# Optimization experiments

Hardware: AMD Instinct MI355X
Metric: run time of the kernel (lower is better)

The kernel has to match this reference:

```python
import jax, jax.numpy as jnp
import numpy as np

PI = np.float32(np.pi)


def _normal(v):
    return v / jnp.linalg.norm(v, axis=-1, keepdims=True)


def camera_mats(cameras):
    # cameras: [V,5] -> rotation matrices c: [V,3,3], camera origins o: [V,3]
    theta = cameras[:, 0] * (PI / 180.0)
    phi = cameras[:, 1] * (PI / 180.0)
    camy = cameras[:, 3] * jnp.sin(phi)
    lens = cameras[:, 3] * jnp.cos(phi)
    camx = lens * jnp.cos(theta)
    camz = lens * jnp.sin(theta)
    Zax = jnp.stack([camx, camy, camz], -1)                                   # [V,3]
    Yax = jnp.stack([camy * jnp.cos(theta + PI), lens, camy * jnp.sin(theta + PI)], -1)
    Xax = jnp.cross(Yax, Zax)
    c = jnp.stack([_normal(Xax), _normal(Yax), _normal(Zax)], axis=1)         # [V,3,3]
    return c, Zax


def setup_inputs() -> dict:
    key = jax.random.key(0)
    k0, k1, k2, k3, k4, k5 = jax.random.split(key, 6)
    N = 65536
    return {
        "inputs": jax.random.normal(k0, (N, 3), jnp.float32),
        "cameras": jax.random.uniform(k1, (3, 5), jnp.float32),
        "feat0": jax.random.normal(k2, (3, 64, 56, 56), jnp.float32),
        "feat1": jax.random.normal(k3, (3, 128, 28, 28), jnp.float32),
        "feat2": jax.random.normal(k4, (3, 256, 14, 14), jnp.float32),
        "feat3": jax.random.normal(k5, (3, 512, 7, 7), jnp.float32),
    }


def reference(inputs, cameras, feat0, feat1, feat2, feat3):
    V = 3
    N = inputs.shape[0]
    c, o = camera_mats(cameras)                      # [V,3,3], [V,3]
    # camera_trans_inv with view 0: xyz @ inv(c0.T) + o0
    point_origin = inputs @ jnp.linalg.inv(c[0].T) + o[0]          # [N,3]
    # camera_trans per view: (p - o_v) @ c_v.T
    pts = jnp.einsum('vnd,vkd->vnk', point_origin[None, :, :] - o[:, None, :], c)  # [V,N,3]
    X, Y, Z = pts[..., 0], pts[..., 1], pts[..., 2]
    h = jnp.clip(jnp.nan_to_num(248.0 * (-Y) / (-Z) + 112.0), 0.0, 223.0)
    w = jnp.clip(jnp.nan_to_num(248.0 * X / (-Z) + 112.0), 0.0, 223.0)
    n = jnp.broadcast_to(jnp.arange(V, dtype=jnp.float32)[:, None], (V, N))
    indices = jnp.stack([n, h, w], axis=-1)                        # [V,N,3] float

    def gather(feat, size):
        # faithful: n is also divided and truncated -> batch index always 0
        idx = (indices / (224.0 / size)).astype(jnp.int32)         # [V,N,3]
        f = jnp.transpose(feat, (0, 2, 3, 1))                      # [B,H,W,C]
        return f[idx[..., 0], idx[..., 1], idx[..., 2]]            # [V,N,C]

    image_feature = jnp.concatenate(
        [gather(feat0, 56.0), gather(feat1, 28.0), gather(feat2, 14.0), gather(feat3, 7.0)],
        axis=2)                                                    # [V,N,960]
    fmax = jnp.max(image_feature, axis=0)
    fmean = jnp.mean(image_feature, axis=0)
    fstd = jnp.sqrt(jnp.mean((image_feature - fmean) ** 2, axis=0))  # biased std
    return jnp.concatenate([inputs, fmax, fmean, fstd], axis=1)    # [N, 3+3*960]
```

## Files before the change

kernel.cpp:

```cpp
#include <hip/hip_runtime.h>
#include <math.h>


#define TBL_TOTAL 376320
#define TBL_OFF0  0
#define TBL_OFF1  200704
#define TBL_OFF2  301056
#define TBL_OFF3  351232

__device__ __forceinline__ void compute_cams(const float* __restrict__ cams,
                                             double M[3][3], double o0[3],
                                             double cm[3][3][3], double om[3][3]) {
  const double DEG  = (double)(3.14159274101257324f / 180.0f);
  const double PI_D = (double)3.14159274101257324f;
  for (int v = 0; v < 3; ++v) {
    double th = (double)cams[v * 5 + 0] * DEG;
    double ph = (double)cams[v * 5 + 1] * DEG;
    double dd = (double)cams[v * 5 + 3];
    double camy = dd * sin(ph);
    double lens = dd * cos(ph);
    double camx = lens * cos(th);
    double camz = lens * sin(th);
    double Zx = camx, Zy = camy, Zz = camz;
    double Yx = camy * cos(th + PI_D), Yy = lens, Yz = camy * sin(th + PI_D);
    double Xx = Yy * Zz - Yz * Zy;
    double Xy = Yz * Zx - Yx * Zz;
    double Xz = Yx * Zy - Yy * Zx;
    double nX = sqrt(Xx * Xx + Xy * Xy + Xz * Xz);
    double nY = sqrt(Yx * Yx + Yy * Yy + Yz * Yz);
    double nZ = sqrt(Zx * Zx + Zy * Zy + Zz * Zz);
    cm[v][0][0] = Xx / nX; cm[v][0][1] = Xy / nX; cm[v][0][2] = Xz / nX;
    cm[v][1][0] = Yx / nY; cm[v][1][1] = Yy / nY; cm[v][1][2] = Yz / nY;
    cm[v][2][0] = Zx / nZ; cm[v][2][1] = Zy / nZ; cm[v][2][2] = Zz / nZ;
    om[v][0] = Zx; om[v][1] = Zy; om[v][2] = Zz;
  }
  double a00 = cm[0][0][0], a01 = cm[0][1][0], a02 = cm[0][2][0];
  double a10 = cm[0][0][1], a11 = cm[0][1][1], a12 = cm[0][2][1];
  double a20 = cm[0][0][2], a21 = cm[0][1][2], a22 = cm[0][2][2];
  double det = a00 * (a11 * a22 - a12 * a21)
             - a01 * (a10 * a22 - a12 * a20)
             + a02 * (a10 * a21 - a11 * a20);
  M[0][0] = (a11 * a22 - a12 * a21) / det;
  M[0][1] = (a02 * a21 - a01 * a22) / det;
  M[0][2] = (a01 * a12 - a02 * a11) / det;
  M[1][0] = (a12 * a20 - a10 * a22) / det;
  M[1][1] = (a00 * a22 - a02 * a20) / det;
  M[1][2] = (a02 * a10 - a00 * a12) / det;
  M[2][0] = (a10 * a21 - a11 * a20) / det;
  M[2][1] = (a01 * a20 - a00 * a21) / det;
  M[2][2] = (a00 * a11 - a01 * a10) / det;
  o0[0] = om[0][0]; o0[1] = om[0][1]; o0[2] = om[0][2];
}

__global__ void k_setup(const float* __restrict__ cams, double* __restrict__ P) {
  if (threadIdx.x != 0 || blockIdx.x != 0) return;
  double M[3][3], o0[3], cm[3][3][3], om[3][3];
  compute_cams(cams, M, o0, cm, om);
  int i = 0;
  for (int r = 0; r < 3; ++r)
    for (int k = 0; k < 3; ++k) P[i++] = M[r][k];
  for (int k = 0; k < 3; ++k) P[i++] = o0[k];
  for (int v = 0; v < 3; ++v)
    for (int r = 0; r < 3; ++r)
      for (int k = 0; k < 3; ++k) P[i++] = cm[v][r][k];
  for (int v = 0; v < 3; ++v)
    for (int k = 0; k < 3; ++k) P[i++] = om[v][k];
}

__global__ void k_transpose(const float* __restrict__ f0, const float* __restrict__ f1,
                            const float* __restrict__ f2, const float* __restrict__ f3,
                            float* __restrict__ tbl) {
  int i = blockIdx.x * 256 + threadIdx.x;
  if (i >= TBL_TOTAL) return;
  const float* src;
  int j, cmask, clog, HW;
  if (i < TBL_OFF1)      { src = f0; j = i;            cmask = 63;  clog = 6; HW = 3136; }
  else if (i < TBL_OFF2) { src = f1; j = i - TBL_OFF1; cmask = 127; clog = 7; HW = 784;  }
  else if (i < TBL_OFF3) { src = f2; j = i - TBL_OFF2; cmask = 255; clog = 8; HW = 196;  }
  else                   { src = f3; j = i - TBL_OFF3; cmask = 511; clog = 9; HW = 49;   }
  int c  = j & cmask;
  int hw = j >> clog;
  tbl[i] = src[c * HW + hw];
}

template <bool TRANSPOSED>
__global__ __launch_bounds__(256) void k_main(
    const float* __restrict__ inpts, const float* __restrict__ cams,
    const double* __restrict__ P, const float* __restrict__ tbl,
    const float* __restrict__ f0, const float* __restrict__ f1,
    const float* __restrict__ f2, const float* __restrict__ f3,
    float* __restrict__ out) {
  __shared__ int s_off[3][4];
  const int p = blockIdx.x;
  const int tid = threadIdx.x;

  if (tid < 3) {
    const int v = tid;
    double M[3][3], o0[3], cmv[3][3], ovv[3];
    if (TRANSPOSED) {
      M[0][0] = P[0]; M[0][1] = P[1]; M[0][2] = P[2];
      M[1][0] = P[3]; M[1][1] = P[4]; M[1][2] = P[5];
      M[2][0] = P[6]; M[2][1] = P[7]; M[2][2] = P[8];
      o0[0] = P[9]; o0[1] = P[10]; o0[2] = P[11];
      for (int r = 0; r < 3; ++r)
        for (int k = 0; k < 3; ++k) cmv[r][k] = P[12 + v * 9 + r * 3 + k];
      ovv[0] = P[39 + v * 3 + 0]; ovv[1] = P[39 + v * 3 + 1]; ovv[2] = P[39 + v * 3 + 2];
    } else {
      double cm[3][3][3], om[3][3];
      compute_cams(cams, M, o0, cm, om);
      for (int r = 0; r < 3; ++r)
        for (int k = 0; k < 3; ++k) cmv[r][k] = cm[v][r][k];
      ovv[0] = om[v][0]; ovv[1] = om[v][1]; ovv[2] = om[v][2];
    }
    double x = (double)inpts[p * 3 + 0];
    double y = (double)inpts[p * 3 + 1];
    double z = (double)inpts[p * 3 + 2];
    double p0 = x * M[0][0] + y * M[1][0] + z * M[2][0] + o0[0];
    double p1 = x * M[0][1] + y * M[1][1] + z * M[2][1] + o0[1];
    double p2 = x * M[0][2] + y * M[1][2] + z * M[2][2] + o0[2];
    double q0 = p0 - ovv[0], q1 = p1 - ovv[1], q2 = p2 - ovv[2];
    double Xc = q0 * cmv[0][0] + q1 * cmv[0][1] + q2 * cmv[0][2];
    double Yc = q0 * cmv[1][0] + q1 * cmv[1][1] + q2 * cmv[1][2];
    double Zc = q0 * cmv[2][0] + q1 * cmv[2][1] + q2 * cmv[2][2];
    double nz = -Zc;
    double hv = 248.0 * (-Yc) / nz + 112.0;
    double wv = 248.0 * Xc / nz + 112.0;
    if (isnan(hv)) hv = 0.0;
    if (isnan(wv)) wv = 0.0;
    hv = fmin(fmax(hv, 0.0), 223.0);
    wv = fmin(fmax(wv, 0.0), 223.0);
    int h0 = (int)(hv * 0.25),    w0 = (int)(wv * 0.25);
    int h1 = (int)(hv * 0.125),   w1 = (int)(wv * 0.125);
    int h2 = (int)(hv * 0.0625),  w2 = (int)(wv * 0.0625);
    int h3 = (int)(hv * 0.03125), w3 = (int)(wv * 0.03125);
    if (TRANSPOSED) {
      s_off[v][0] = TBL_OFF0 + (h0 * 56 + w0) * 64;
      s_off[v][1] = TBL_OFF1 + (h1 * 28 + w1) * 128;
      s_off[v][2] = TBL_OFF2 + (h2 * 14 + w2) * 256;
      s_off[v][3] = TBL_OFF3 + (h3 * 7  + w3) * 512;
    } else {
      s_off[v][0] = h0 * 56 + w0;
      s_off[v][1] = h1 * 28 + w1;
      s_off[v][2] = h2 * 14 + w2;
      s_off[v][3] = h3 * 7  + w3;
    }
    out[p * 2883 + v] = inpts[p * 3 + v];
  }
  __syncthreads();

  const int row = p * 2883;
  for (int c = tid; c < 960; c += 256) {
    int l, cl;
    if (c < 64)       { l = 0; cl = c; }
    else if (c < 192) { l = 1; cl = c - 64; }
    else if (c < 448) { l = 2; cl = c - 192; }
    else              { l = 3; cl = c - 448; }
    float v0, v1, v2;
    if (TRANSPOSED) {
      v0 = tbl[s_off[0][l] + cl];
      v1 = tbl[s_off[1][l] + cl];
      v2 = tbl[s_off[2][l] + cl];
    } else {
      const float* f = (l == 0) ? f0 : (l == 1) ? f1 : (l == 2) ? f2 : f3;
      const int HW   = (l == 0) ? 3136 : (l == 1) ? 784 : (l == 2) ? 196 : 49;
      v0 = f[cl * HW + s_off[0][l]];
      v1 = f[cl * HW + s_off[1][l]];
      v2 = f[cl * HW + s_off[2][l]];
    }
    float mx = fmaxf(fmaxf(v0, v1), v2);
    float sm = (v0 + v1) + v2;
    float mean = sm / 3.0f;
    float d0 = v0 - mean, d1 = v1 - mean, d2 = v2 - mean;
    float var = ((d0 * d0 + d1 * d1) + d2 * d2) / 3.0f;
    float sd = sqrtf(var);
    out[row + 3 + c]    = mx;
    out[row + 963 + c]  = mean;
    out[row + 1923 + c] = sd;
  }
}

extern "C" void kernel_launch(void* const* d_in, const int* in_sizes, int n_in,
                              void* d_out, int out_size, void* d_ws, size_t ws_size,
                              hipStream_t stream) {
  const float* inpts = (const float*)d_in[0];
  const float* cams  = (const float*)d_in[1];
  const float* f0    = (const float*)d_in[2];
  const float* f1    = (const float*)d_in[3];
  const float* f2    = (const float*)d_in[4];
  const float* f3    = (const float*)d_in[5];
  float* out = (float*)d_out;
  const int N = in_sizes[0] / 3;

  const size_t TBL_BYTE_OFF = 512;
  const size_t NEED = TBL_BYTE_OFF + (size_t)TBL_TOTAL * sizeof(float);

  if (ws_size >= NEED) {
    double* P  = (double*)d_ws;
    float* tbl = (float*)((char*)d_ws + TBL_BYTE_OFF);
    k_setup<<<1, 64, 0, stream>>>(cams, P);
    k_transpose<<<(TBL_TOTAL + 255) / 256, 256, 0, stream>>>(f0, f1, f2, f3, tbl);
    k_main<true><<<N, 256, 0, stream>>>(inpts, cams, P, tbl, f0, f1, f2, f3, out);
  } else {
    k_main<false><<<N, 256, 0, stream>>>(inpts, cams, nullptr, nullptr, f0, f1, f2, f3, out);
  }
}
```

Baseline: 830.0 us.

## Split projection into its own kernel and gather one point per wavefront

Moves the per-point camera projection into a separate kernel that computes all three views per thread and writes table offsets to workspace. The gather kernel then processes four points per block, one wavefront each, with a fully unrolled 15-iteration channel loop and no shared memory or barrier. This removes the per-block serial projection by three threads and the __syncthreads that stalled the gather. The cost is an extra kernel launch, an offsets buffer round trip through memory, and a larger workspace requirement that may push execution onto the fallback path.

```diff
diff --git a/kernel.cpp b/kernel.cpp
--- a/kernel.cpp
+++ b/kernel.cpp
@@ -83,99 +83,144 @@
   tbl[i] = src[c * HW + hw];
 }
 
-template <bool TRANSPOSED>
-__global__ __launch_bounds__(256) void k_main(
+__global__ __launch_bounds__(256) void k_proj(const float* __restrict__ inpts,
+                                              const double* __restrict__ P,
+                                              int* __restrict__ offs,
+                                              float* __restrict__ out, int N) {
+  const int p = blockIdx.x * 256 + threadIdx.x;
+  if (p >= N) return;
+
+  const double x = (double)inpts[p * 3 + 0];
+  const double y = (double)inpts[p * 3 + 1];
+  const double z = (double)inpts[p * 3 + 2];
+
+  const double p0 = x * P[0] + y * P[3] + z * P[6] + P[9];
+  const double p1 = x * P[1] + y * P[4] + z * P[7] + P[10];
+  const double p2 = x * P[2] + y * P[5] + z * P[8] + P[11];
+
+  #pragma unroll
+  for (int v = 0; v < 3; ++v) {
+    const double q0 = p0 - P[39 + v * 3 + 0];
+    const double q1 = p1 - P[39 + v * 3 + 1];
+    const double q2 = p2 - P[39 + v * 3 + 2];
+    const int cb = 12 + v * 9;
+    const double Xc = q0 * P[cb + 0] + q1 * P[cb + 1] + q2 * P[cb + 2];
+    const double Yc = q0 * P[cb + 3] + q1 * P[cb + 4] + q2 * P[cb + 5];
+    const double Zc = q0 * P[cb + 6] + q1 * P[cb + 7] + q2 * P[cb + 8];
+    const double nz = -Zc;
+    double hv = 248.0 * (-Yc) / nz + 112.0;
+    double wv = 248.0 * Xc / nz + 112.0;
+    if (isnan(hv)) hv = 0.0;
+    if (isnan(wv)) wv = 0.0;
+    hv = fmin(fmax(hv, 0.0), 223.0);
+    wv = fmin(fmax(wv, 0.0), 223.0);
+    const int h0 = (int)(hv * 0.25),    w0 = (int)(wv * 0.25);
+    const int h1 = (int)(hv * 0.125),   w1 = (int)(wv * 0.125);
+    const int h2 = (int)(hv * 0.0625),  w2 = (int)(wv * 0.0625);
+    const int h3 = (int)(hv * 0.03125), w3 = (int)(wv * 0.03125);
+    offs[p * 12 + v * 4 + 0] = TBL_OFF0 + (h0 * 56 + w0) * 64;
+    offs[p * 12 + v * 4 + 1] = TBL_OFF1 + (h1 * 28 + w1) * 128;
+    offs[p * 12 + v * 4 + 2] = TBL_OFF2 + (h2 * 14 + w2) * 256;
+    offs[p * 12 + v * 4 + 3] = TBL_OFF3 + (h3 * 7  + w3) * 512;
+  }
+  out[(size_t)p * 2883 + 0] = (float)x;
+  out[(size_t)p * 2883 + 1] = (float)y;
+  out[(size_t)p * 2883 + 2] = (float)z;
+}
+
+__global__ __launch_bounds__(256) void k_gather(const int* __restrict__ offs,
+                                                const float* __restrict__ tbl,
+                                                float* __restrict__ out, int N) {
+  const int lane = threadIdx.x & 63;
+  const int wv   = threadIdx.x >> 6;
+  const int p    = blockIdx.x * 4 + wv;
+  if (p >= N) return;
+
+  const int4* ob = (const int4*)(offs + p * 12);
+  const int4 oa = ob[0], obb = ob[1], oc = ob[2];
+  const int o_[3][4] = {{oa.x, oa.y, oa.z, oa.w},
+                        {obb.x, obb.y, obb.z, obb.w},
+                        {oc.x, oc.y, oc.z, oc.w}};
+
+  float* op = out + (size_t)p * 2883;
+
+  #pragma unroll
+  for (int it = 0; it < 15; ++it) {
+    const int c  = it * 64 + lane;
+    const int l  = (it < 1) ? 0 : (it < 3) ? 1 : (it < 7) ? 2 : 3;
+    const int cb = (l == 0) ? 0 : (l == 1) ? 64 : (l == 2) ? 192 : 448;
+    const int cl = c - cb;
+    const float v0 = tbl[o_[0][l] + cl];
+    const float v1 = tbl[o_[1][l] + cl];
+    const float v2 = tbl[o_[2][l] + cl];
+    const float mx   = fmaxf(fmaxf(v0, v1), v2);
+    const float sm   = (v0 + v1) + v2;
+    const float mean = sm / 3.0f;
+    const float d0 = v0 - mean, d1 = v1 - mean, d2 = v2 - mean;
+    const float var = ((d0 * d0 + d1 * d1) + d2 * d2) / 3.0f;
+    const float sd = sqrtf(var);
+    op[3 + c]    = mx;
+    op[963 + c]  = mean;
+    op[1923 + c] = sd;
+  }
+}
+
+__global__ __launch_bounds__(256) void k_main_fallback(
     const float* __restrict__ inpts, const float* __restrict__ cams,
-    const double* __restrict__ P, const float* __restrict__ tbl,
     const float* __restrict__ f0, const float* __restrict__ f1,
     const float* __restrict__ f2, const float* __restrict__ f3,
     float* __restrict__ out) {
   __shared__ int s_off[3][4];
   const int p = blockIdx.x;
   const int tid = threadIdx.x;
-
   if (tid < 3) {
     const int v = tid;
-    double M[3][3], o0[3], cmv[3][3], ovv[3];
-    if (TRANSPOSED) {
-      M[0][0] = P[0]; M[0][1] = P[1]; M[0][2] = P[2];
-      M[1][0] = P[3]; M[1][1] = P[4]; M[1][2] = P[5];
-      M[2][0] = P[6]; M[2][1] = P[7]; M[2][2] = P[8];
-      o0[0] = P[9]; o0[1] = P[10]; o0[2] = P[11];
-      for (int r = 0; r < 3; ++r)
-        for (int k = 0; k < 3; ++k) cmv[r][k] = P[12 + v * 9 + r * 3 + k];
-      ovv[0] = P[39 + v * 3 + 0]; ovv[1] = P[39 + v * 3 + 1]; ovv[2] = P[39 + v * 3 + 2];
-    } else {
-      double cm[3][3][3], om[3][3];
-      compute_cams(cams, M, o0, cm, om);
-      for (int r = 0; r < 3; ++r)
-        for (int k = 0; k < 3; ++k) cmv[r][k] = cm[v][r][k];
-      ovv[0] = om[v][0]; ovv[1] = om[v][1]; ovv[2] = om[v][2];
-    }
+    double M[3][3], o0[3], cm[3][3][3], om[3][3];
+    compute_cams(cams, M, o0, cm, om);
     double x = (double)inpts[p * 3 + 0];
     double y = (double)inpts[p * 3 + 1];
     double z = (double)inpts[p * 3 + 2];
     double p0 = x * M[0][0] + y * M[1][0] + z * M[2][0] + o0[0];
     double p1 = x * M[0][1] + y * M[1][1] + z * M[2][1] + o0[1];
     double p2 = x * M[0][2] + y * M[1][2] + z * M[2][2] + o0[2];
-    double q0 = p0 - ovv[0], q1 = p1 - ovv[1], q2 = p2 - ovv[2];
-    double Xc = q0 * cmv[0][0] + q1 * cmv[0][1] + q2 * cmv[0][2];
-    double Yc = q0 * cmv[1][0] + q1 * cmv[1][1] + q2 * cmv[1][2];
-    double Zc = q0 * cmv[2][0] + q1 * cmv[2][1] + q2 * cmv[2][2];
+    double q0 = p0 - om[v][0], q1 = p1 - om[v][1], q2 = p2 - om[v][2];
+    double Xc = q0 * cm[v][0][0] + q1 * cm[v][0][1] + q2 * cm[v][0][2];
+    double Yc = q0 * cm[v][1][0] + q1 * cm[v][1][1] + q2 * cm[v][1][2];
+    double Zc = q0 * cm[v][2][0] + q1 * cm[v][2][1] + q2 * cm[v][2][2];
     double nz = -Zc;
     double hv = 248.0 * (-Yc) / nz + 112.0;
-    double wv = 248.0 * Xc / nz + 112.0;
+    double wv2 = 248.0 * Xc / nz + 112.0;
     if (isnan(hv)) hv = 0.0;
-    if (isnan(wv)) wv = 0.0;
+    if (isnan(wv2)) wv2 = 0.0;
     hv = fmin(fmax(hv, 0.0), 223.0);
-    wv = fmin(fmax(wv, 0.0), 223.0);
-    int h0 = (int)(hv * 0.25),    w0 = (int)(wv * 0.25);
-    int h1 = (int)(hv * 0.125),   w1 = (int)(wv * 0.125);
-    int h2 = (int)(hv * 0.0625),  w2 = (int)(wv * 0.0625);
-    int h3 = (int)(hv * 0.03125), w3 = (int)(wv * 0.03125);
-    if (TRANSPOSED) {
-      s_off[v][0] = TBL_OFF0 + (h0 * 56 + w0) * 64;
-      s_off[v][1] = TBL_OFF1 + (h1 * 28 + w1) * 128;
-      s_off[v][2] = TBL_OFF2 + (h2 * 14 + w2) * 256;
-      s_off[v][3] = TBL_OFF3 + (h3 * 7  + w3) * 512;
-    } else {
-      s_off[v][0] = h0 * 56 + w0;
-      s_off[v][1] = h1 * 28 + w1;
-      s_off[v][2] = h2 * 14 + w2;
-      s_off[v][3] = h3 * 7  + w3;
-    }
-    out[p * 2883 + v] = inpts[p * 3 + v];
+    wv2 = fmin(fmax(wv2, 0.0), 223.0);
+    s_off[v][0] = (int)(hv * 0.25)    * 56 + (int)(wv2 * 0.25);
+    s_off[v][1] = (int)(hv * 0.125)   * 28 + (int)(wv2 * 0.125);
+    s_off[v][2] = (int)(hv * 0.0625)  * 14 + (int)(wv2 * 0.0625);
+    s_off[v][3] = (int)(hv * 0.03125) * 7  + (int)(wv2 * 0.03125);
+    out[(size_t)p * 2883 + v] = inpts[p * 3 + v];
   }
   __syncthreads();
-
-  const int row = p * 2883;
+  const size_t row = (size_t)p * 2883;
   for (int c = tid; c < 960; c += 256) {
     int l, cl;
     if (c < 64)       { l = 0; cl = c; }
     else if (c < 192) { l = 1; cl = c - 64; }
     else if (c < 448) { l = 2; cl = c - 192; }
     else              { l = 3; cl = c - 448; }
-    float v0, v1, v2;
-    if (TRANSPOSED) {
-      v0 = tbl[s_off[0][l] + cl];
-      v1 = tbl[s_off[1][l] + cl];
-      v2 = tbl[s_off[2][l] + cl];
-    } else {
-      const float* f = (l == 0) ? f0 : (l == 1) ? f1 : (l == 2) ? f2 : f3;
-      const int HW   = (l == 0) ? 3136 : (l == 1) ? 784 : (l == 2) ? 196 : 49;
-      v0 = f[cl * HW + s_off[0][l]];
-      v1 = f[cl * HW + s_off[1][l]];
-      v2 = f[cl * HW + s_off[2][l]];
-    }
+    const float* f = (l == 0) ? f0 : (l == 1) ? f1 : (l == 2) ? f2 : f3;
+    const int HW   = (l == 0) ? 3136 : (l == 1) ? 784 : (l == 2) ? 196 : 49;
+    float v0 = f[cl * HW + s_off[0][l]];
+    float v1 = f[cl * HW + s_off[1][l]];
+    float v2 = f[cl * HW + s_off[2][l]];
     float mx = fmaxf(fmaxf(v0, v1), v2);
     float sm = (v0 + v1) + v2;
     float mean = sm / 3.0f;
     float d0 = v0 - mean, d1 = v1 - mean, d2 = v2 - mean;
     float var = ((d0 * d0 + d1 * d1) + d2 * d2) / 3.0f;
-    float sd = sqrtf(var);
     out[row + 3 + c]    = mx;
     out[row + 963 + c]  = mean;
-    out[row + 1923 + c] = sd;
+    out[row + 1923 + c] = sqrtf(var);
   }
 }
 
@@ -191,16 +236,20 @@
   float* out = (float*)d_out;
   const int N = in_sizes[0] / 3;
 
-  const size_t TBL_BYTE_OFF = 512;
-  const size_t NEED = TBL_BYTE_OFF + (size_t)TBL_TOTAL * sizeof(float);
+  const size_t P_OFF    = 0;
+  const size_t TBL_BOFF = 512;
+  const size_t OFF_BOFF = TBL_BOFF + (size_t)TBL_TOTAL * sizeof(float);
+  const size_t NEED     = OFF_BOFF + (size_t)N * 12 * sizeof(int);
 
   if (ws_size >= NEED) {
-    double* P  = (double*)d_ws;
-    float* tbl = (float*)((char*)d_ws + TBL_BYTE_OFF);
+    double* P  = (double*)((char*)d_ws + P_OFF);
+    float* tbl = (float*)((char*)d_ws + TBL_BOFF);
+    int* offs  = (int*)((char*)d_ws + OFF_BOFF);
     k_setup<<<1, 64, 0, stream>>>(cams, P);
     k_transpose<<<(TBL_TOTAL + 255) / 256, 256, 0, stream>>>(f0, f1, f2, f3, tbl);
-    k_main<true><<<N, 256, 0, stream>>>(inpts, cams, P, tbl, f0, f1, f2, f3, out);
+    k_proj<<<(N + 255) / 256, 256, 0, stream>>>(inpts, P, offs, out, N);
+    k_gather<<<(N + 3) / 4, 256, 0, stream>>>(offs, tbl, out, N);
   } else {
-    k_main<false><<<N, 256, 0, stream>>>(inpts, cams, nullptr, nullptr, f0, f1, f2, f3, out);
-  }
-}
+    k_main_fallback<<<N, 256, 0, stream>>>(inpts, cams, f0, f1, f2, f3, out);
+  }
+}
```

After: 830.2 us. Within noise of the previous version (+0.0%).
